# Optimization experiments

Hardware: AMD Instinct MI355X
Metric: run time of the kernel (lower is better)

The kernel has to match this reference:

```python
import jax, jax.numpy as jnp
import numpy as np

BETA = 0.1


def setup_inputs() -> dict:
    key = jax.random.key(0)
    ks = jax.random.split(key, 8)
    B, S, H, V = 4, 512, 2048, 32000
    return {
        "lin_weight": jax.random.normal(ks[0], (V, H), jnp.float32) * 0.02,
        "_input": jax.random.normal(ks[1], (B, S, H), jnp.float32),
        "attention_mask": jnp.ones((B, S), jnp.float32),
        "rewards": jax.random.normal(ks[2], (B,), jnp.float32),
        "bias": jax.random.normal(ks[3], (V,), jnp.float32) * 0.02,
        "ref_input": jax.random.normal(ks[4], (B, S, H), jnp.float32),
        "ref_weight": jax.random.normal(ks[5], (V, H), jnp.float32) * 0.02,
        "ref_bias": jax.random.normal(ks[6], (V,), jnp.float32) * 0.02,
    }


def _seq_logps(x, w, b, mask):
    # logits: [B,S,V]; per-token max log-softmax, masked, summed over seq
    logits = jnp.einsum("bsh,vh->bsv", x, w) + b
    lp = jax.nn.log_softmax(logits, axis=-1)
    seq = (jnp.max(lp, axis=-1) * mask).sum(axis=-1)  # [B]
    return logits, seq


def reference(lin_weight, _input, attention_mask, rewards, bias, ref_input, ref_weight, ref_bias):
    policy_logits, seq_log_probs = _seq_logps(_input, lin_weight, bias, attention_mask)
    _, ref_seq_logps = _seq_logps(ref_input, ref_weight, ref_bias, attention_mask)
    ref_seq_logps = jax.lax.stop_gradient(ref_seq_logps)

    adv = rewards - rewards.mean()
    std = jnp.std(rewards, ddof=1)  # torch unbiased std
    adv = jnp.where(std > 0, adv / std, adv)

    kl_div = seq_log_probs - ref_seq_logps
    loss = (-(adv * seq_log_probs) + BETA * kl_div).mean()

    metrics = (
        seq_log_probs.mean(),
        jnp.std(seq_log_probs, ddof=1),
        policy_logits.mean(),
        kl_div.mean(),
    )
    return (loss,) + metrics
```

## Files before the change

### kernel.cpp

```cpp
#include <hip/hip_runtime.h>
#include <hip/hip_fp16.h>
#include <math.h>

#define TOK 2048
#define HD 2048
#define VOC 32000
#define BM 256
#define BN 256
#define BK 64
#define NT (HD/BK)
#define NCH (VOC/64)
#define NBLK ((TOK/BM)*(VOC/BN))

typedef _Float16 half8 __attribute__((ext_vector_type(8)));
typedef float float4v __attribute__((ext_vector_type(4)));

#define GLB __attribute__((address_space(1)))
#define LDSAS __attribute__((address_space(3)))

static __device__ __forceinline__ void gload_lds16(const void* g, void* l) {
  __builtin_amdgcn_global_load_lds((const GLB unsigned int*)g,
                                   (LDSAS unsigned int*)l, 16, 0, 0);
}

static __device__ __forceinline__ float4v mfma16(half8 a, half8 b, float4v c) {
  return __builtin_amdgcn_mfma_f32_16x16x32_f16(a, b, c, 0, 0, 0);
}

__global__ void cvt_f32_f16(const float* __restrict__ in,
                            _Float16* __restrict__ out, int n8) {
  for (int i = blockIdx.x * blockDim.x + threadIdx.x; i < n8;
       i += gridDim.x * blockDim.x) {
    float4v a = *(const float4v*)(in + (size_t)i*8);
    float4v b = *(const float4v*)(in + (size_t)i*8 + 4);
    half8 h;
    #pragma unroll
    for (int j=0;j<4;j++) { h[j] = (_Float16)a[j]; h[4+j] = (_Float16)b[j]; }
    *(half8*)(out + (size_t)i*8) = h;
  }
}

template<int CB, bool SG1, bool SG2, int VMN>
__device__ __forceinline__ void ktile(
    unsigned char* ldsby, const char* Xb, const char* Wb,
    int sA0, int sA1, int sB0, int sB1, int ldst0, int ldst1, int kbn,
    const int (&aofs)[8], const int (&bofs)[4], float4v (&acc)[8][4])
{
  constexpr int U0 = CB, U1 = CB + 16384, U2 = CB + 32768, U3 = CB + 49152;
  half8 af1[8], bf1[4], af2lo[4], bf2[4], af2hi[4];

  #pragma unroll
  for (int n=0;n<4;n++) bf1[n] = *(const half8*)(ldsby + U1 + bofs[n]);
  #pragma unroll
  for (int m=0;m<8;m++) af1[m] = *(const half8*)(ldsby + U0 + aofs[m]);
  if (SG1) {
    gload_lds16(Xb + (sA0 + kbn + 64), ldsby + ((CB^65536) + 32768) + ldst0);
    gload_lds16(Xb + (sA1 + kbn + 64), ldsby + ((CB^65536) + 32768) + ldst1);
    gload_lds16(Wb + (sB0 + kbn + 64), ldsby + ((CB^65536) + 49152) + ldst0);
    gload_lds16(Wb + (sB1 + kbn + 64), ldsby + ((CB^65536) + 49152) + ldst1);
  }
  __builtin_amdgcn_s_setprio(1);
  #pragma unroll
  for (int m=0;m<4;m++)
    #pragma unroll
    for (int n=0;n<4;n++)
      acc[m][n] = mfma16(af1[m], bf1[n], acc[m][n]);
  #pragma unroll
  for (int n=0;n<4;n++) bf2[n]   = *(const half8*)(ldsby + U3 + bofs[n]);
  #pragma unroll
  for (int m=0;m<4;m++) af2lo[m] = *(const half8*)(ldsby + U2 + aofs[m]);
  #pragma unroll
  for (int m=4;m<8;m++)
    #pragma unroll
    for (int n=0;n<4;n++)
      acc[m][n] = mfma16(af1[m], bf1[n], acc[m][n]);
  __builtin_amdgcn_s_setprio(0);
  __builtin_amdgcn_s_barrier();

  #pragma unroll
  for (int m=0;m<4;m++) af2hi[m] = *(const half8*)(ldsby + U2 + aofs[4+m]);
  if (SG2) {
    gload_lds16(Xb + (sA0 + kbn + 128), ldsby + (CB + 0)     + ldst0);
    gload_lds16(Xb + (sA1 + kbn + 128), ldsby + (CB + 0)     + ldst1);
    gload_lds16(Wb + (sB0 + kbn + 128), ldsby + (CB + 16384) + ldst0);
    gload_lds16(Wb + (sB1 + kbn + 128), ldsby + (CB + 16384) + ldst1);
  }
  __builtin_amdgcn_s_setprio(1);
  #pragma unroll
  for (int m=0;m<4;m++)
    #pragma unroll
    for (int n=0;n<4;n++)
      acc[m][n] = mfma16(af2lo[m], bf2[n], acc[m][n]);
  #pragma unroll
  for (int m=0;m<4;m++)
    #pragma unroll
    for (int n=0;n<4;n++)
      acc[4+m][n] = mfma16(af2hi[m], bf2[n], acc[4+m][n]);
  __builtin_amdgcn_s_setprio(0);
  if (VMN == 4)      asm volatile("s_waitcnt vmcnt(4)" ::: "memory");
  else if (VMN == 0) asm volatile("s_waitcnt vmcnt(0)" ::: "memory");
  __builtin_amdgcn_s_barrier();
}

__global__ __launch_bounds__(512, 2) void gemm_stats_f16(
    const _Float16* __restrict__ Xh, const _Float16* __restrict__ Wh,
    const float* __restrict__ bias,
    float* __restrict__ pmax, float* __restrict__ psum,
    float* __restrict__ bsum, int computeSum)
{
  __shared__ unsigned char ldsbuf[131072];
  unsigned char* ldsby = ldsbuf;

  int bid = blockIdx.x;
  int swz = (bid & 7) * (NBLK/8) + (bid >> 3);
  int rowt = swz & 7;
  int colt = swz >> 3;
  int brow = rowt * BM;
  int bcol = colt * BN;

  int tid  = threadIdx.x;
  int lane = tid & 63;
  int wv   = tid >> 6;
  int wr   = wv >> 2;
  int wc   = wv & 3;
  int l15  = lane & 15;
  int q    = lane >> 4;

  int aswz = (((((l15 & 1) << 2) | q) ^ ((l15 >> 1) & 7)) << 4) + ((l15 >> 1) << 7);
  int aofs[8], bofs[4];
  #pragma unroll
  for (int m = 0; m < 8; m++) aofs[m] = wr*8192 + m*1024 + aswz;
  #pragma unroll
  for (int n = 0; n < 4; n++) bofs[n] = wc*4096 + n*1024 + aswz;

  int s8  = (tid & 7) ^ ((tid >> 3) & 7);
  int rl  = wv*16 + (((tid >> 3) & 7) << 1) + (s8 >> 2);
  int kc  = (s8 & 3) << 4;
  int sA0 = (brow + rl)*(HD*2) + kc;
  int sA1 = sA0 + 128*(HD*2);
  int sB0 = (bcol + rl)*(HD*2) + kc;
  int sB1 = sB0 + 128*(HD*2);
  int ldst0 = (wv << 10);
  int ldst1 = (wv << 10) + 8192;

  const char* Xb = (const char*)Xh;
  const char* Wb = (const char*)Wh;

  float4v acc[8][4];
  #pragma unroll
  for (int m=0;m<8;m++)
    #pragma unroll
    for (int n=0;n<4;n++) acc[m][n] = (float4v){0.f,0.f,0.f,0.f};

  gload_lds16(Xb + sA0,       ldsby + 0     + ldst0);
  gload_lds16(Xb + sA1,       ldsby + 0     + ldst1);
  gload_lds16(Wb + sB0,       ldsby + 16384 + ldst0);
  gload_lds16(Wb + sB1,       ldsby + 16384 + ldst1);
  gload_lds16(Xb + (sA0+64),  ldsby + 32768 + ldst0);
  gload_lds16(Xb + (sA1+64),  ldsby + 32768 + ldst1);
  gload_lds16(Wb + (sB0+64),  ldsby + 49152 + ldst0);
  gload_lds16(Wb + (sB1+64),  ldsby + 49152 + ldst1);
  gload_lds16(Xb + (sA0+128), ldsby + 65536 + ldst0);
  gload_lds16(Xb + (sA1+128), ldsby + 65536 + ldst1);
  gload_lds16(Wb + (sB0+128), ldsby + 81920 + ldst0);
  gload_lds16(Wb + (sB1+128), ldsby + 81920 + ldst1);
  asm volatile("s_waitcnt vmcnt(4)" ::: "memory");
  __builtin_amdgcn_s_barrier();

  int kbn = 128;
  #pragma unroll 1
  for (int i = 0; i < 15; ++i) {
    ktile<0,     true, true, 4>(ldsby, Xb, Wb, sA0,sA1,sB0,sB1, ldst0,ldst1, kbn, aofs, bofs, acc);
    kbn += 128;
    ktile<65536, true, true, 4>(ldsby, Xb, Wb, sA0,sA1,sB0,sB1, ldst0,ldst1, kbn, aofs, bofs, acc);
    kbn += 128;
  }
  ktile<0,     true,  false, 0>(ldsby, Xb, Wb, sA0,sA1,sB0,sB1, ldst0,ldst1, kbn, aofs, bofs, acc);
  kbn += 128;
  ktile<65536, false, false, -1>(ldsby, Xb, Wb, sA0,sA1,sB0,sB1, ldst0,ldst1, kbn, aofs, bofs, acc);

  float bv[4];
  #pragma unroll
  for (int n=0;n<4;n++) bv[n] = bias[bcol + wc*64 + n*16 + l15];

  float lsum = 0.f;
  int ch = colt*4 + wc;
  #pragma unroll
  for (int m=0;m<8;m++) {
    #pragma unroll
    for (int r=0;r<4;r++) {
      float v0 = acc[m][0][r] + bv[0];
      float v1 = acc[m][1][r] + bv[1];
      float v2 = acc[m][2][r] + bv[2];
      float v3 = acc[m][3][r] + bv[3];
      if (computeSum) lsum += v0+v1+v2+v3;
      float mx = fmaxf(fmaxf(v0,v1), fmaxf(v2,v3));
      #pragma unroll
      for (int off=1; off<16; off<<=1) mx = fmaxf(mx, __shfl_xor(mx, off, 64));
      float se = __expf(v0-mx)+__expf(v1-mx)+__expf(v2-mx)+__expf(v3-mx);
      #pragma unroll
      for (int off=1; off<16; off<<=1) se += __shfl_xor(se, off, 64);
      if (l15 == 0) {
        int row = brow + wr*128 + m*16 + (lane>>4)*4 + r;
        pmax[(size_t)row*NCH + ch] = mx;
        psum[(size_t)row*NCH + ch] = se;
      }
    }
  }

  if (computeSum) {
    #pragma unroll
    for (int off=1; off<64; off<<=1) lsum += __shfl_xor(lsum, off, 64);
    __syncthreads();
    float* red = (float*)ldsbuf;
    if (lane == 0) red[wv] = lsum;
    __syncthreads();
    if (tid == 0) {
      float s = 0.f;
      for (int w=0; w<8; w++) s += red[w];
      bsum[blockIdx.x] = s;
    }
  }
}

__global__ void row_combine(const float* __restrict__ pmax,
                            const float* __restrict__ psum,
                            const float* __restrict__ mask,
                            float* __restrict__ tok)
{
  int row = blockIdx.x;
  int lane = threadIdx.x;
  float M = -INFINITY;
  for (int c = lane; c < NCH; c += 64) M = fmaxf(M, pmax[(size_t)row*NCH + c]);
  #pragma unroll
  for (int off=1; off<64; off<<=1) M = fmaxf(M, __shfl_xor(M, off, 64));
  float L = 0.f;
  for (int c = lane; c < NCH; c += 64)
    L += psum[(size_t)row*NCH + c] * __expf(pmax[(size_t)row*NCH + c] - M);
  #pragma unroll
  for (int off=1; off<64; off<<=1) L += __shfl_xor(L, off, 64);
  if (lane == 0) tok[row] = -logf(L) * mask[row];
}

__global__ void finalize(const float* __restrict__ tokP,
                         const float* __restrict__ tokR,
                         const float* __restrict__ rewards,
                         const float* __restrict__ bsum, int nbsum,
                         float* __restrict__ out)
{
  __shared__ float red[256];
  __shared__ float seqP[4], seqR[4];
  int t = threadIdx.x;
  for (int b=0; b<4; b++) {
    float v = tokP[b*512 + t] + tokP[b*512 + 256 + t];
    red[t] = v; __syncthreads();
    for (int s=128; s>0; s>>=1) { if (t < s) red[t] += red[t+s]; __syncthreads(); }
    if (t == 0) seqP[b] = red[0];
    __syncthreads();
    v = tokR[b*512 + t] + tokR[b*512 + 256 + t];
    red[t] = v; __syncthreads();
    for (int s=128; s>0; s>>=1) { if (t < s) red[t] += red[t+s]; __syncthreads(); }
    if (t == 0) seqR[b] = red[0];
    __syncthreads();
  }
  float ls = 0.f;
  for (int i=t; i<nbsum; i+=256) ls += bsum[i];
  red[t] = ls; __syncthreads();
  for (int s=128; s>0; s>>=1) { if (t < s) red[t] += red[t+s]; __syncthreads(); }
  if (t == 0) {
    float r0=rewards[0], r1=rewards[1], r2=rewards[2], r3=rewards[3];
    float rm = (r0+r1+r2+r3)*0.25f;
    float var = ((r0-rm)*(r0-rm)+(r1-rm)*(r1-rm)+(r2-rm)*(r2-rm)+(r3-rm)*(r3-rm))/3.f;
    float rstd = sqrtf(var);
    float adv[4] = {r0-rm, r1-rm, r2-rm, r3-rm};
    if (rstd > 0.f) { for (int b=0;b<4;b++) adv[b] /= rstd; }
    float loss=0.f, sm=0.f, km=0.f;
    for (int b=0;b<4;b++) {
      float kl = seqP[b] - seqR[b];
      loss += -(adv[b]*seqP[b]) + 0.1f*kl;
      sm += seqP[b]; km += kl;
    }
    loss *= 0.25f; sm *= 0.25f; km *= 0.25f;
    float sv = 0.f;
    for (int b=0;b<4;b++) { float d = seqP[b]-sm; sv += d*d; }
    float sstd = sqrtf(sv/3.f);
    out[0] = loss;
    out[1] = sm;
    out[2] = sstd;
    out[3] = red[0] / ((float)TOK * (float)VOC);
    out[4] = km;
  }
}

extern "C" void kernel_launch(void* const* d_in, const int* in_sizes, int n_in,
                              void* d_out, int out_size, void* d_ws, size_t ws_size,
                              hipStream_t stream) {
  const float* W    = (const float*)d_in[0];
  const float* X    = (const float*)d_in[1];
  const float* mask = (const float*)d_in[2];
  const float* rew  = (const float*)d_in[3];
  const float* bias = (const float*)d_in[4];
  const float* Xr   = (const float*)d_in[5];
  const float* Wr   = (const float*)d_in[6];
  const float* br   = (const float*)d_in[7];
  float* out = (float*)d_out;

  float* pmax = (float*)d_ws;
  float* psum = pmax + (size_t)TOK*NCH;
  float* tokP = psum + (size_t)TOK*NCH;
  float* tokR = tokP + TOK;
  float* bsum = tokR + TOK;

  size_t headFloats = (size_t)TOK*NCH*2 + TOK*2 + 4096;
  size_t offXh = headFloats * 4;
  _Float16* Xh = (_Float16*)((unsigned char*)d_ws + offXh);
  _Float16* Wh = (_Float16*)((unsigned char*)d_ws + offXh + (size_t)TOK*HD*2);

  cvt_f32_f16<<<2048, 256, 0, stream>>>(X,  Xh, TOK*HD/8);
  cvt_f32_f16<<<2048, 256, 0, stream>>>(W,  Wh, VOC*HD/8);
  gemm_stats_f16<<<NBLK, 512, 0, stream>>>(Xh, Wh, bias, pmax, psum, bsum, 1);
  row_combine<<<TOK, 64, 0, stream>>>(pmax, psum, mask, tokP);
  cvt_f32_f16<<<2048, 256, 0, stream>>>(Xr, Xh, TOK*HD/8);
  cvt_f32_f16<<<2048, 256, 0, stream>>>(Wr, Wh, VOC*HD/8);
  gemm_stats_f16<<<NBLK, 512, 0, stream>>>(Xh, Wh, br, pmax, psum, bsum, 0);
  row_combine<<<TOK, 64, 0, stream>>>(pmax, psum, mask, tokR);
  finalize<<<1, 256, 0, stream>>>(tokP, tokR, rew, bsum, NBLK, out);
}
```

Baseline: 678.5 us.

## Fuse reference weight fp16 conversion into policy GEMM main loop

Folds the f32-to-f16 conversion of the reference weight matrix into the first GEMM kernel. Each block converts its share of that matrix in slices interleaved with its k-tiles, loading a slice in one tile and storing it in the next, so the conversion's memory traffic hides under MFMA compute instead of running as a separate bandwidth-bound launch. The reference activations and weights get their own workspace buffers so the second GEMM does not overwrite the first. This path needs a larger workspace and falls back to the old sequence otherwise. It adds register pressure and global traffic inside the GEMM loop, which may slow the first GEMM.

```diff
diff --git a/kernel.cpp b/kernel.cpp
--- a/kernel.cpp
+++ b/kernel.cpp
@@ -11,6 +11,8 @@
 #define NT (HD/BK)
 #define NCH (VOC/64)
 #define NBLK ((TOK/BM)*(VOC/BN))
+#define NGW (VOC*HD/8)
+#define GPBW (NGW/NBLK)
 
 typedef _Float16 half8 __attribute__((ext_vector_type(8)));
 typedef float float4v __attribute__((ext_vector_type(4)));
@@ -40,19 +42,34 @@
   }
 }
 
-template<int CB, bool SG1, bool SG2, int VMN>
+template<int CB, bool SG1, bool SG2, bool EMB, int VMN>
 __device__ __forceinline__ void ktile(
     unsigned char* ldsby, const char* Xb, const char* Wb,
     int sA0, int sA1, int sB0, int sB1, int ldst0, int ldst1, int kbn,
-    const int (&aofs)[8], const int (&bofs)[4], float4v (&acc)[8][4])
+    const int (&aofs)[8], const int (&bofs)[4], float4v (&acc)[8][4],
+    const float* __restrict__ csrc, _Float16* __restrict__ cdst,
+    int slotPrev, int slotCur, int blkBase, float4v (&cbuf)[2])
 {
-  constexpr int U0 = CB, U1 = CB + 16384, U2 = CB + 32768, U3 = CB + 49152;
   half8 af1[8], bf1[4], af2lo[4], bf2[4], af2hi[4];
 
   #pragma unroll
-  for (int n=0;n<4;n++) bf1[n] = *(const half8*)(ldsby + U1 + bofs[n]);
-  #pragma unroll
-  for (int m=0;m<8;m++) af1[m] = *(const half8*)(ldsby + U0 + aofs[m]);
+  for (int n=0;n<4;n++) bf1[n] = *(const half8*)(ldsby + CB + 16384 + bofs[n]);
+  #pragma unroll
+  for (int m=0;m<8;m++) af1[m] = *(const half8*)(ldsby + CB + aofs[m]);
+  if (EMB) {
+    if (slotPrev >= 0) {
+      int gi = blkBase + slotPrev;
+      half8 h;
+      #pragma unroll
+      for (int j=0;j<4;j++) { h[j] = (_Float16)cbuf[0][j]; h[4+j] = (_Float16)cbuf[1][j]; }
+      *(half8*)(cdst + (size_t)gi*8) = h;
+    }
+    if (slotCur >= 0) {
+      int gi = blkBase + slotCur;
+      cbuf[0] = *(const float4v*)(csrc + (size_t)gi*8);
+      cbuf[1] = *(const float4v*)(csrc + (size_t)gi*8 + 4);
+    }
+  }
   if (SG1) {
     gload_lds16(Xb + (sA0 + kbn + 64), ldsby + ((CB^65536) + 32768) + ldst0);
     gload_lds16(Xb + (sA1 + kbn + 64), ldsby + ((CB^65536) + 32768) + ldst1);
@@ -66,9 +83,9 @@
     for (int n=0;n<4;n++)
       acc[m][n] = mfma16(af1[m], bf1[n], acc[m][n]);
   #pragma unroll
-  for (int n=0;n<4;n++) bf2[n]   = *(const half8*)(ldsby + U3 + bofs[n]);
-  #pragma unroll
-  for (int m=0;m<4;m++) af2lo[m] = *(const half8*)(ldsby + U2 + aofs[m]);
+  for (int n=0;n<4;n++) bf2[n]   = *(const half8*)(ldsby + CB + 49152 + bofs[n]);
+  #pragma unroll
+  for (int m=0;m<4;m++) af2lo[m] = *(const half8*)(ldsby + CB + 32768 + aofs[m]);
   #pragma unroll
   for (int m=4;m<8;m++)
     #pragma unroll
@@ -78,10 +95,10 @@
   __builtin_amdgcn_s_barrier();
 
   #pragma unroll
-  for (int m=0;m<4;m++) af2hi[m] = *(const half8*)(ldsby + U2 + aofs[4+m]);
+  for (int m=0;m<4;m++) af2hi[m] = *(const half8*)(ldsby + CB + 32768 + aofs[4+m]);
   if (SG2) {
-    gload_lds16(Xb + (sA0 + kbn + 128), ldsby + (CB + 0)     + ldst0);
-    gload_lds16(Xb + (sA1 + kbn + 128), ldsby + (CB + 0)     + ldst1);
+    gload_lds16(Xb + (sA0 + kbn + 128), ldsby + CB + ldst0);
+    gload_lds16(Xb + (sA1 + kbn + 128), ldsby + CB + ldst1);
     gload_lds16(Wb + (sB0 + kbn + 128), ldsby + (CB + 16384) + ldst0);
     gload_lds16(Wb + (sB1 + kbn + 128), ldsby + (CB + 16384) + ldst1);
   }
@@ -102,11 +119,13 @@
   __builtin_amdgcn_s_barrier();
 }
 
+template<bool EMB>
 __global__ __launch_bounds__(512, 2) void gemm_stats_f16(
     const _Float16* __restrict__ Xh, const _Float16* __restrict__ Wh,
     const float* __restrict__ bias,
     float* __restrict__ pmax, float* __restrict__ psum,
-    float* __restrict__ bsum, int computeSum)
+    float* __restrict__ bsum, int computeSum,
+    const float* __restrict__ csrc, _Float16* __restrict__ cdst)
 {
   __shared__ unsigned char ldsbuf[131072];
   unsigned char* ldsby = ldsbuf;
@@ -145,6 +164,10 @@
 
   const char* Xb = (const char*)Xh;
   const char* Wb = (const char*)Wh;
+
+  int blkBase = bid * GPBW;
+  float4v cbuf[2];
+  int sofs = tid;
 
   float4v acc[8][4];
   #pragma unroll
@@ -170,14 +193,21 @@
   int kbn = 128;
   #pragma unroll 1
   for (int i = 0; i < 15; ++i) {
-    ktile<0,     true, true, 4>(ldsby, Xb, Wb, sA0,sA1,sB0,sB1, ldst0,ldst1, kbn, aofs, bofs, acc);
+    int t0 = 2*i, t1 = 2*i+1;
+    ktile<0,     true,true,EMB, 4>(ldsby, Xb, Wb, sA0,sA1,sB0,sB1, ldst0,ldst1, kbn,
+        aofs, bofs, acc, csrc, cdst,
+        (t0>=1 && t0<=16) ? (t0-1)*512+sofs : -1, (t0<=15) ? t0*512+sofs : -1, blkBase, cbuf);
     kbn += 128;
-    ktile<65536, true, true, 4>(ldsby, Xb, Wb, sA0,sA1,sB0,sB1, ldst0,ldst1, kbn, aofs, bofs, acc);
+    ktile<65536, true,true,EMB, 4>(ldsby, Xb, Wb, sA0,sA1,sB0,sB1, ldst0,ldst1, kbn,
+        aofs, bofs, acc, csrc, cdst,
+        (t1>=1 && t1<=16) ? (t1-1)*512+sofs : -1, (t1<=15) ? t1*512+sofs : -1, blkBase, cbuf);
     kbn += 128;
   }
-  ktile<0,     true,  false, 0>(ldsby, Xb, Wb, sA0,sA1,sB0,sB1, ldst0,ldst1, kbn, aofs, bofs, acc);
+  ktile<0,     true,false,false, 0>(ldsby, Xb, Wb, sA0,sA1,sB0,sB1, ldst0,ldst1, kbn,
+      aofs, bofs, acc, csrc, cdst, -1, -1, blkBase, cbuf);
   kbn += 128;
-  ktile<65536, false, false, -1>(ldsby, Xb, Wb, sA0,sA1,sB0,sB1, ldst0,ldst1, kbn, aofs, bofs, acc);
+  ktile<65536, false,false,false, -1>(ldsby, Xb, Wb, sA0,sA1,sB0,sB1, ldst0,ldst1, kbn,
+      aofs, bofs, acc, csrc, cdst, -1, -1, blkBase, cbuf);
 
   float bv[4];
   #pragma unroll
@@ -313,16 +343,32 @@
 
   size_t headFloats = (size_t)TOK*NCH*2 + TOK*2 + 4096;
   size_t offXh = headFloats * 4;
-  _Float16* Xh = (_Float16*)((unsigned char*)d_ws + offXh);
-  _Float16* Wh = (_Float16*)((unsigned char*)d_ws + offXh + (size_t)TOK*HD*2);
-
-  cvt_f32_f16<<<2048, 256, 0, stream>>>(X,  Xh, TOK*HD/8);
-  cvt_f32_f16<<<2048, 256, 0, stream>>>(W,  Wh, VOC*HD/8);
-  gemm_stats_f16<<<NBLK, 512, 0, stream>>>(Xh, Wh, bias, pmax, psum, bsum, 1);
-  row_combine<<<TOK, 64, 0, stream>>>(pmax, psum, mask, tokP);
-  cvt_f32_f16<<<2048, 256, 0, stream>>>(Xr, Xh, TOK*HD/8);
-  cvt_f32_f16<<<2048, 256, 0, stream>>>(Wr, Wh, VOC*HD/8);
-  gemm_stats_f16<<<NBLK, 512, 0, stream>>>(Xh, Wh, br, pmax, psum, bsum, 0);
-  row_combine<<<TOK, 64, 0, stream>>>(pmax, psum, mask, tokR);
-  finalize<<<1, 256, 0, stream>>>(tokP, tokR, rew, bsum, NBLK, out);
-}
+  size_t xhB = (size_t)TOK*HD*2, whB = (size_t)VOC*HD*2;
+  unsigned char* wsb = (unsigned char*)d_ws;
+  _Float16* XhP = (_Float16*)(wsb + offXh);
+  _Float16* WhP = (_Float16*)(wsb + offXh + xhB);
+  _Float16* XhR = (_Float16*)(wsb + offXh + xhB + whB);
+  size_t needOverlap = offXh + 2*(xhB + whB);
+
+  if (ws_size >= needOverlap) {
+    _Float16* WhR = XhR + (size_t)TOK*HD;
+    cvt_f32_f16<<<2048, 256, 0, stream>>>(X,  XhP, TOK*HD/8);
+    cvt_f32_f16<<<2048, 256, 0, stream>>>(W,  WhP, VOC*HD/8);
+    gemm_stats_f16<true><<<NBLK, 512, 0, stream>>>(XhP, WhP, bias, pmax, psum, bsum, 1, Wr, WhR);
+    cvt_f32_f16<<<2048, 256, 0, stream>>>(Xr, XhR, TOK*HD/8);
+    row_combine<<<TOK, 64, 0, stream>>>(pmax, psum, mask, tokP);
+    gemm_stats_f16<false><<<NBLK, 512, 0, stream>>>(XhR, WhR, br, pmax, psum, bsum, 0, nullptr, nullptr);
+    row_combine<<<TOK, 64, 0, stream>>>(pmax, psum, mask, tokR);
+    finalize<<<1, 256, 0, stream>>>(tokP, tokR, rew, bsum, NBLK, out);
+  } else {
+    cvt_f32_f16<<<2048, 256, 0, stream>>>(X,  XhP, TOK*HD/8);
+    cvt_f32_f16<<<2048, 256, 0, stream>>>(W,  WhP, VOC*HD/8);
+    gemm_stats_f16<false><<<NBLK, 512, 0, stream>>>(XhP, WhP, bias, pmax, psum, bsum, 1, nullptr, nullptr);
+    row_combine<<<TOK, 64, 0, stream>>>(pmax, psum, mask, tokP);
+    cvt_f32_f16<<<2048, 256, 0, stream>>>(Xr, XhP, TOK*HD/8);
+    cvt_f32_f16<<<2048, 256, 0, stream>>>(Wr, WhP, VOC*HD/8);
+    gemm_stats_f16<false><<<NBLK, 512, 0, stream>>>(XhP, WhP, br, pmax, psum, bsum, 0, nullptr, nullptr);
+    row_combine<<<TOK, 64, 0, stream>>>(pmax, psum, mask, tokR);
+    finalize<<<1, 256, 0, stream>>>(tokP, tokR, rew, bsum, NBLK, out);
+  }
+}
```

New measurement: 725.9 us. +7.0%, slower.

## Shrink GEMM tile to 256x128 with triple-buffered 32-wide K stages

Applied to the files above, without the earlier changes.

Cuts the block's column tile from 256 to 128 and reorganises the main loop into single 32-wide K stages. These stages rotate through three LDS buffers, with one barrier per stage and an explicit lgkmcnt wait before the MFMAs. LDS use drops from 128 KB to 72 KB, each wave holds a 4x4 accumulator grid instead of 8x4, and the launch-bounds target rises to 4 blocks per CU. The aim is higher occupancy and less register and LDS pressure. In exchange each block reuses its data less, global traffic per FLOP goes up, and there are more barriers per unit of work.

```diff
diff --git a/kernel.cpp b/kernel.cpp
--- a/kernel.cpp
+++ b/kernel.cpp
@@ -6,8 +6,8 @@
 #define HD 2048
 #define VOC 32000
 #define BM 256
-#define BN 256
-#define BK 64
+#define BN 128
+#define BK 32
 #define NT (HD/BK)
 #define NCH (VOC/64)
 #define NBLK ((TOK/BM)*(VOC/BN))
@@ -40,75 +40,44 @@
   }
 }
 
-template<int CB, bool SG1, bool SG2, int VMN>
-__device__ __forceinline__ void ktile(
+template<int BUF, bool SG, int VM>
+__device__ __forceinline__ void ktile32(
     unsigned char* ldsby, const char* Xb, const char* Wb,
-    int sA0, int sA1, int sB0, int sB1, int ldst0, int ldst1, int kbn,
-    const int (&aofs)[8], const int (&bofs)[4], float4v (&acc)[8][4])
-{
-  constexpr int U0 = CB, U1 = CB + 16384, U2 = CB + 32768, U3 = CB + 49152;
-  half8 af1[8], bf1[4], af2lo[4], bf2[4], af2hi[4];
-
-  #pragma unroll
-  for (int n=0;n<4;n++) bf1[n] = *(const half8*)(ldsby + U1 + bofs[n]);
-  #pragma unroll
-  for (int m=0;m<8;m++) af1[m] = *(const half8*)(ldsby + U0 + aofs[m]);
-  if (SG1) {
-    gload_lds16(Xb + (sA0 + kbn + 64), ldsby + ((CB^65536) + 32768) + ldst0);
-    gload_lds16(Xb + (sA1 + kbn + 64), ldsby + ((CB^65536) + 32768) + ldst1);
-    gload_lds16(Wb + (sB0 + kbn + 64), ldsby + ((CB^65536) + 49152) + ldst0);
-    gload_lds16(Wb + (sB1 + kbn + 64), ldsby + ((CB^65536) + 49152) + ldst1);
-  }
+    int sA0, int sA1, int sB, int ldstA0, int ldstA1, int ldstB, int kbn,
+    const int (&aofs)[4], const int (&bofs)[4], float4v (&acc)[4][4])
+{
+  constexpr int SGBUF = (BUF + 49152) % 73728;
+  half8 af[4], bf[4];
+  #pragma unroll
+  for (int m=0;m<4;m++) af[m] = *(const half8*)(ldsby + BUF + aofs[m]);
+  #pragma unroll
+  for (int n=0;n<4;n++) bf[n] = *(const half8*)(ldsby + BUF + 16384 + bofs[n]);
+  if (SG) {
+    gload_lds16(Xb + (sA0 + kbn), ldsby + SGBUF + ldstA0);
+    gload_lds16(Xb + (sA1 + kbn), ldsby + SGBUF + ldstA1);
+    gload_lds16(Wb + (sB  + kbn), ldsby + SGBUF + 16384 + ldstB);
+  }
+  if (VM == 3)      asm volatile("s_waitcnt vmcnt(3)" ::: "memory");
+  else if (VM == 0) asm volatile("s_waitcnt vmcnt(0)" ::: "memory");
+  __builtin_amdgcn_s_barrier();
+  asm volatile("s_waitcnt lgkmcnt(0)" ::: "memory");
+  __builtin_amdgcn_sched_barrier(0);
   __builtin_amdgcn_s_setprio(1);
   #pragma unroll
   for (int m=0;m<4;m++)
     #pragma unroll
     for (int n=0;n<4;n++)
-      acc[m][n] = mfma16(af1[m], bf1[n], acc[m][n]);
-  #pragma unroll
-  for (int n=0;n<4;n++) bf2[n]   = *(const half8*)(ldsby + U3 + bofs[n]);
-  #pragma unroll
-  for (int m=0;m<4;m++) af2lo[m] = *(const half8*)(ldsby + U2 + aofs[m]);
-  #pragma unroll
-  for (int m=4;m<8;m++)
-    #pragma unroll
-    for (int n=0;n<4;n++)
-      acc[m][n] = mfma16(af1[m], bf1[n], acc[m][n]);
+      acc[m][n] = mfma16(af[m], bf[n], acc[m][n]);
   __builtin_amdgcn_s_setprio(0);
-  __builtin_amdgcn_s_barrier();
-
-  #pragma unroll
-  for (int m=0;m<4;m++) af2hi[m] = *(const half8*)(ldsby + U2 + aofs[4+m]);
-  if (SG2) {
-    gload_lds16(Xb + (sA0 + kbn + 128), ldsby + (CB + 0)     + ldst0);
-    gload_lds16(Xb + (sA1 + kbn + 128), ldsby + (CB + 0)     + ldst1);
-    gload_lds16(Wb + (sB0 + kbn + 128), ldsby + (CB + 16384) + ldst0);
-    gload_lds16(Wb + (sB1 + kbn + 128), ldsby + (CB + 16384) + ldst1);
-  }
-  __builtin_amdgcn_s_setprio(1);
-  #pragma unroll
-  for (int m=0;m<4;m++)
-    #pragma unroll
-    for (int n=0;n<4;n++)
-      acc[m][n] = mfma16(af2lo[m], bf2[n], acc[m][n]);
-  #pragma unroll
-  for (int m=0;m<4;m++)
-    #pragma unroll
-    for (int n=0;n<4;n++)
-      acc[4+m][n] = mfma16(af2hi[m], bf2[n], acc[4+m][n]);
-  __builtin_amdgcn_s_setprio(0);
-  if (VMN == 4)      asm volatile("s_waitcnt vmcnt(4)" ::: "memory");
-  else if (VMN == 0) asm volatile("s_waitcnt vmcnt(0)" ::: "memory");
-  __builtin_amdgcn_s_barrier();
-}
-
-__global__ __launch_bounds__(512, 2) void gemm_stats_f16(
+}
+
+__global__ __launch_bounds__(512, 4) void gemm_stats_f16(
     const _Float16* __restrict__ Xh, const _Float16* __restrict__ Wh,
     const float* __restrict__ bias,
     float* __restrict__ pmax, float* __restrict__ psum,
     float* __restrict__ bsum, int computeSum)
 {
-  __shared__ unsigned char ldsbuf[131072];
+  __shared__ unsigned char ldsbuf[73728];
   unsigned char* ldsby = ldsbuf;
 
   int bid = blockIdx.x;
@@ -121,15 +90,15 @@
   int tid  = threadIdx.x;
   int lane = tid & 63;
   int wv   = tid >> 6;
-  int wr   = wv >> 2;
-  int wc   = wv & 3;
+  int wr   = wv >> 1;
+  int wc   = wv & 1;
   int l15  = lane & 15;
   int q    = lane >> 4;
 
   int aswz = (((((l15 & 1) << 2) | q) ^ ((l15 >> 1) & 7)) << 4) + ((l15 >> 1) << 7);
-  int aofs[8], bofs[4];
-  #pragma unroll
-  for (int m = 0; m < 8; m++) aofs[m] = wr*8192 + m*1024 + aswz;
+  int aofs[4], bofs[4];
+  #pragma unroll
+  for (int m = 0; m < 4; m++) aofs[m] = wr*4096 + m*1024 + aswz;
   #pragma unroll
   for (int n = 0; n < 4; n++) bofs[n] = wc*4096 + n*1024 + aswz;
 
@@ -138,55 +107,49 @@
   int kc  = (s8 & 3) << 4;
   int sA0 = (brow + rl)*(HD*2) + kc;
   int sA1 = sA0 + 128*(HD*2);
-  int sB0 = (bcol + rl)*(HD*2) + kc;
-  int sB1 = sB0 + 128*(HD*2);
-  int ldst0 = (wv << 10);
-  int ldst1 = (wv << 10) + 8192;
+  int sB  = (bcol + rl)*(HD*2) + kc;
+  int ldstA0 = (wv << 10);
+  int ldstA1 = (wv << 10) + 8192;
+  int ldstB  = (wv << 10);
 
   const char* Xb = (const char*)Xh;
   const char* Wb = (const char*)Wh;
 
-  float4v acc[8][4];
-  #pragma unroll
-  for (int m=0;m<8;m++)
+  float4v acc[4][4];
+  #pragma unroll
+  for (int m=0;m<4;m++)
     #pragma unroll
     for (int n=0;n<4;n++) acc[m][n] = (float4v){0.f,0.f,0.f,0.f};
 
-  gload_lds16(Xb + sA0,       ldsby + 0     + ldst0);
-  gload_lds16(Xb + sA1,       ldsby + 0     + ldst1);
-  gload_lds16(Wb + sB0,       ldsby + 16384 + ldst0);
-  gload_lds16(Wb + sB1,       ldsby + 16384 + ldst1);
-  gload_lds16(Xb + (sA0+64),  ldsby + 32768 + ldst0);
-  gload_lds16(Xb + (sA1+64),  ldsby + 32768 + ldst1);
-  gload_lds16(Wb + (sB0+64),  ldsby + 49152 + ldst0);
-  gload_lds16(Wb + (sB1+64),  ldsby + 49152 + ldst1);
-  gload_lds16(Xb + (sA0+128), ldsby + 65536 + ldst0);
-  gload_lds16(Xb + (sA1+128), ldsby + 65536 + ldst1);
-  gload_lds16(Wb + (sB0+128), ldsby + 81920 + ldst0);
-  gload_lds16(Wb + (sB1+128), ldsby + 81920 + ldst1);
-  asm volatile("s_waitcnt vmcnt(4)" ::: "memory");
+  gload_lds16(Xb + sA0,      ldsby + 0     + ldstA0);
+  gload_lds16(Xb + sA1,      ldsby + 0     + ldstA1);
+  gload_lds16(Wb + sB,       ldsby + 16384 + ldstB);
+  gload_lds16(Xb + (sA0+64), ldsby + 24576 + ldstA0);
+  gload_lds16(Xb + (sA1+64), ldsby + 24576 + ldstA1);
+  gload_lds16(Wb + (sB+64),  ldsby + 40960 + ldstB);
+  asm volatile("s_waitcnt vmcnt(3)" ::: "memory");
   __builtin_amdgcn_s_barrier();
 
   int kbn = 128;
   #pragma unroll 1
-  for (int i = 0; i < 15; ++i) {
-    ktile<0,     true, true, 4>(ldsby, Xb, Wb, sA0,sA1,sB0,sB1, ldst0,ldst1, kbn, aofs, bofs, acc);
-    kbn += 128;
-    ktile<65536, true, true, 4>(ldsby, Xb, Wb, sA0,sA1,sB0,sB1, ldst0,ldst1, kbn, aofs, bofs, acc);
-    kbn += 128;
-  }
-  ktile<0,     true,  false, 0>(ldsby, Xb, Wb, sA0,sA1,sB0,sB1, ldst0,ldst1, kbn, aofs, bofs, acc);
-  kbn += 128;
-  ktile<65536, false, false, -1>(ldsby, Xb, Wb, sA0,sA1,sB0,sB1, ldst0,ldst1, kbn, aofs, bofs, acc);
+  for (int i = 0; i < 20; ++i) {
+    ktile32<0,     true, 3>(ldsby, Xb, Wb, sA0,sA1,sB, ldstA0,ldstA1,ldstB, kbn, aofs, bofs, acc); kbn += 64;
+    ktile32<24576, true, 3>(ldsby, Xb, Wb, sA0,sA1,sB, ldstA0,ldstA1,ldstB, kbn, aofs, bofs, acc); kbn += 64;
+    ktile32<49152, true, 3>(ldsby, Xb, Wb, sA0,sA1,sB, ldstA0,ldstA1,ldstB, kbn, aofs, bofs, acc); kbn += 64;
+  }
+  ktile32<0,     true,  3>(ldsby, Xb, Wb, sA0,sA1,sB, ldstA0,ldstA1,ldstB, kbn, aofs, bofs, acc); kbn += 64;
+  ktile32<24576, true,  3>(ldsby, Xb, Wb, sA0,sA1,sB, ldstA0,ldstA1,ldstB, kbn, aofs, bofs, acc); kbn += 64;
+  ktile32<49152, false, 0>(ldsby, Xb, Wb, sA0,sA1,sB, ldstA0,ldstA1,ldstB, kbn, aofs, bofs, acc);
+  ktile32<0,     false,-1>(ldsby, Xb, Wb, sA0,sA1,sB, ldstA0,ldstA1,ldstB, kbn, aofs, bofs, acc);
 
   float bv[4];
   #pragma unroll
   for (int n=0;n<4;n++) bv[n] = bias[bcol + wc*64 + n*16 + l15];
 
   float lsum = 0.f;
-  int ch = colt*4 + wc;
-  #pragma unroll
-  for (int m=0;m<8;m++) {
+  int ch = colt*2 + wc;
+  #pragma unroll
+  for (int m=0;m<4;m++) {
     #pragma unroll
     for (int r=0;r<4;r++) {
       float v0 = acc[m][0][r] + bv[0];
@@ -201,7 +164,7 @@
       #pragma unroll
       for (int off=1; off<16; off<<=1) se += __shfl_xor(se, off, 64);
       if (l15 == 0) {
-        int row = brow + wr*128 + m*16 + (lane>>4)*4 + r;
+        int row = brow + wr*64 + m*16 + (lane>>4)*4 + r;
         pmax[(size_t)row*NCH + ch] = mx;
         psum[(size_t)row*NCH + ch] = se;
       }
```

Result: slower. 713.9 us (+5.2%).
